# Performance work log

Measured on AMD Instinct MI355X. Metric: run time of the kernel, lower is better.

The kernel has to match this reference:

```python
import jax, jax.numpy as jnp
import numpy as np

P, H, T, B = 16, 24, 168, 4096


def _lstm(x, W_ih, W_hh, b_ih, b_hh):
    # x: [B, T, F]; PyTorch gate order i, f, g, o; returns all hidden states [B, T, H]
    Bsz = x.shape[0]
    Hd = W_hh.shape[1]
    # batch the input GEMM over all timesteps
    xg = jnp.einsum('btf,gf->btg', x, W_ih) + b_ih + b_hh  # [B, T, 4H]

    def step(carry, xt):
        h, c = carry
        g = xt + h @ W_hh.T  # [B, 4H]
        i, f, gg, o = jnp.split(g, 4, axis=-1)
        c = jax.nn.sigmoid(f) * c + jax.nn.sigmoid(i) * jnp.tanh(gg)
        h = jax.nn.sigmoid(o) * jnp.tanh(c)
        return (h, c), h

    h0 = jnp.zeros((Bsz, Hd), x.dtype)
    _, hs = jax.lax.scan(step, (h0, h0), jnp.swapaxes(xg, 0, 1))
    return jnp.swapaxes(hs, 0, 1)  # [B, T, H]


def setup_inputs() -> dict:
    key = jax.random.key(0)
    ks = jax.random.split(key, 14)
    s1 = 1.0 / np.sqrt(H)
    u = lambda k, shape: jax.random.uniform(k, shape, jnp.float32, -s1, s1)
    return {
        'x': jax.random.normal(ks[0], (B, T, P), jnp.float32),
        'W_ih1': u(ks[1], (4 * H, P)), 'W_hh1': u(ks[2], (4 * H, H)),
        'b_ih1': u(ks[3], (4 * H,)), 'b_hh1': u(ks[4], (4 * H,)),
        'W_ih2': u(ks[5], (4 * H, H)), 'W_hh2': u(ks[6], (4 * H, H)),
        'b_ih2': u(ks[7], (4 * H,)), 'b_hh2': u(ks[8], (4 * H,)),
        'W1': u(ks[9], (16, H)), 'b1': u(ks[10], (16,)),
        'W2': u(ks[11], (H, 16)), 'b2': u(ks[12], (H,)),
    }


def reference(x, W_ih1, W_hh1, b_ih1, b_hh1, W_ih2, W_hh2, b_ih2, b_hh2, W1, b1, W2, b2):
    h = jnp.tanh(_lstm(x, W_ih1, W_hh1, b_ih1, b_hh1))       # [B, T, H]
    h = jnp.tanh(_lstm(h, W_ih2, W_hh2, b_ih2, b_hh2))       # [B, T, H]
    h = h[:, -1, :]                                           # [B, H]
    h = jax.nn.relu(h @ W1.T + b1)                            # [B, 16]; dropout = identity (eval mode)
    out = h @ W2.T + b2                                       # [B, 24]
    return out.reshape(out.shape[0], -1, 1)                   # [B, 24, 1]
```

## Files before the change

kernel.cpp:

```cpp
#include <hip/hip_runtime.h>

constexpr int T = 168;
constexpr int P = 16;
constexpr int H = 24;

typedef float v2f __attribute__((ext_vector_type(2)));

__device__ __forceinline__ v2f mk2(float a, float b) { v2f r; r[0] = a; r[1] = b; return r; }
__device__ __forceinline__ v2f bc2(float a)          { v2f r; r[0] = a; r[1] = a; return r; }
__device__ __forceinline__ v2f pkfma(v2f a, v2f b, v2f c) {
    return __builtin_elementwise_fma(a, b, c);
}

__device__ __forceinline__ float rcp_f(float x) { return __builtin_amdgcn_rcpf(x); }
__device__ __forceinline__ float sigm_f(float x) { return rcp_f(1.f + __expf(-x)); }
__device__ __forceinline__ float tanh_fast(float x) {
    return fmaf(2.f, rcp_f(1.f + __expf(-2.f * x)), -1.f);
}

#define KEEP2(v) asm volatile("" : "+v"(v))
#define LDS_SYNC() asm volatile("s_waitcnt lgkmcnt(0)" ::: "memory")

#define PK4(acc_, v4_, w_, b_) do {                       \
    acc_ = pkfma(bc2((v4_).x), (w_)[(b_)],     acc_);     \
    acc_ = pkfma(bc2((v4_).y), (w_)[(b_) + 1], acc_);     \
    acc_ = pkfma(bc2((v4_).z), (w_)[(b_) + 2], acc_);     \
    acc_ = pkfma(bc2((v4_).w), (w_)[(b_) + 3], acc_); } while (0)

__device__ __forceinline__ void act_store(v2f g, int lane, int half,
                                          float& c, float* hdst, float* tdst)
{
    float a0 = sigm_f(g[0]);
    float px = (half == 0) ? g[1] + g[1] : g[1];
    float sv = sigm_f(px);
    float a1 = (half == 0) ? sv + sv - 1.f : sv;
    float fa = __shfl(a0, lane + 24);
    float oa = __shfl(a1, lane + 24);
    c = fmaf(fa, c, a0 * a1);
    float hv = oa * tanh_fast(c);
    if (tdst) {
        float th = tanh_fast(hv);
        if (lane < H) { hdst[lane] = hv; tdst[lane] = th; }
    } else {
        if (lane < H) hdst[lane] = hv;
    }
}

#define L1_STEP_L(xlsrow_, hrow_, c_, tdst_) do {                      \
    v2f g_ = bias;                                                     \
    _Pragma("unroll")                                                  \
    for (int j_ = 0; j_ < P / 4; ++j_) {                               \
        float4 v_ = ((const float4*)(xlsrow_))[j_];                    \
        PK4(g_, v_, w, 4 * j_);                                        \
    }                                                                  \
    _Pragma("unroll")                                                  \
    for (int k_ = 0; k_ < H / 4; ++k_) {                               \
        float4 hv_ = ((const float4*)(hrow_))[k_];                     \
        PK4(g_, hv_, w, H + 4 * k_);                                   \
    }                                                                  \
    act_store(g_, lane, half, c_, hrow_, tdst_);                       \
} while (0)

#define L2_STEP(trow_, hrow_, c_) do {                                 \
    v2f f_ = bias;                                                     \
    _Pragma("unroll")                                                  \
    for (int k_ = 0; k_ < H / 4; ++k_) {                               \
        float4 tv_ = ((const float4*)(trow_))[k_];                     \
        PK4(f_, tv_, w, 4 * k_);                                       \
    }                                                                  \
    _Pragma("unroll")                                                  \
    for (int k_ = 0; k_ < H / 4; ++k_) {                               \
        float4 hv_ = ((const float4*)(hrow_))[k_];                     \
        PK4(f_, hv_, w, H + 4 * k_);                                   \
    }                                                                  \
    act_store(f_, lane, half, c_, hrow_, nullptr);                     \
} while (0)

__global__ __attribute__((amdgpu_flat_work_group_size(128, 128),
                          amdgpu_num_vgpr(128)))
void lstm2_split6(const float* __restrict__ x,
                  const float* __restrict__ Wih1, const float* __restrict__ Whh1,
                  const float* __restrict__ bih1, const float* __restrict__ bhh1,
                  const float* __restrict__ Wih2, const float* __restrict__ Whh2,
                  const float* __restrict__ bih2, const float* __restrict__ bhh2,
                  const float* __restrict__ W1, const float* __restrict__ b1,
                  const float* __restrict__ W2, const float* __restrict__ b2,
                  float* __restrict__ out)
{
    const int tid  = threadIdx.x;
    const int wid  = tid >> 6;
    const int lane = tid & 63;
    const int s    = (lane < 48) ? lane : 47;
    const int u    = s % H;
    const int half = s / H;
    const int q0   = half * H + u;
    const int q1   = (2 + half) * H + u;
    const int rowA = blockIdx.x * 2;
    const int rowB = rowA + 1;

    const float* __restrict__ Wi = wid ? Wih2 : Wih1;
    const float* __restrict__ Wh = wid ? Whh2 : Whh1;
    const float* __restrict__ bi = wid ? bih2 : bih1;
    const float* __restrict__ bh = wid ? bhh2 : bhh1;
    const int nin = wid ? H : P;

    v2f w[48];
    #pragma unroll
    for (int k = 0; k < H; ++k)
        w[k] = (k < nin) ? mk2(Wi[q0 * nin + k], Wi[q1 * nin + k]) : bc2(0.f);
    #pragma unroll
    for (int k = 0; k < H; ++k)
        w[H + k] = mk2(Wh[q0 * H + k], Wh[q1 * H + k]);
    v2f bias = mk2(bi[q0] + bh[q0], bi[q1] + bh[q1]);

    #pragma unroll
    for (int k = 0; k < 48; ++k) KEEP2(w[k]);
    KEEP2(bias);

    __shared__ __align__(16) float h1s[2][32];
    __shared__ __align__(16) float t1s[2][2][2][32];
    __shared__ __align__(16) float h2s[2][32];
    __shared__ __align__(16) float xls[2][2][8][16];

    const float* __restrict__ xA = x + (size_t)rowA * T * P;
    const float* __restrict__ xB = x + (size_t)rowB * T * P;

    float cA = 0.f, cB = 0.f;

    const int xr  = lane >> 5;
    const int xo4 = lane & 31;
    const float* __restrict__ xbase = xr ? xB : xA;
    float4 xst;

    if (wid == 0) {
        xst = ((const float4*)xbase)[xo4];
        ((float4*)xls[0][xr])[xo4] = xst;
        xst = ((const float4*)(xbase + 128))[xo4];
        LDS_SYNC();

        {
            v2f g = bias;
            #pragma unroll
            for (int j = 0; j < P / 4; ++j) {
                float4 v = ((const float4*)xls[0][0][0])[j];
                PK4(g, v, w, 4 * j);
            }
            act_store(g, lane, half, cA, h1s[0], t1s[0][0][0]);
        }
        {
            v2f g = bias;
            #pragma unroll
            for (int j = 0; j < P / 4; ++j) {
                float4 v = ((const float4*)xls[0][1][0])[j];
                PK4(g, v, w, 4 * j);
            }
            act_store(g, lane, half, cB, h1s[1], t1s[0][0][1]);
        }
        LDS_SYNC();
        L1_STEP_L(xls[0][0][1], h1s[0], cA, t1s[0][1][0]);
        L1_STEP_L(xls[0][1][1], h1s[1], cB, t1s[0][1][1]);
    } else {
        if (lane < H) { h2s[0][lane] = 0.f; h2s[1][lane] = 0.f; }
    }
    LDS_SYNC();
    __builtin_amdgcn_s_barrier();

    for (int ss = 1; ss < T / 2; ++ss) {
        if (wid == 0) {
            if ((ss & 3) == 0) {
                const int ci = ss >> 2;
                ((float4*)xls[ci & 1][xr])[xo4] = xst;
                if (ci < 20)
                    xst = ((const float4*)(xbase + (ci + 1) * 128))[xo4];
                LDS_SYNC();
            }
            const int xb = (ss >> 2) & 1;
            const int ta = 2 * ss;
            L1_STEP_L(xls[xb][0][ta & 7],       h1s[0], cA, t1s[ss & 1][0][0]);
            L1_STEP_L(xls[xb][1][ta & 7],       h1s[1], cB, t1s[ss & 1][0][1]);
            LDS_SYNC();
            L1_STEP_L(xls[xb][0][(ta + 1) & 7], h1s[0], cA, t1s[ss & 1][1][0]);
            L1_STEP_L(xls[xb][1][(ta + 1) & 7], h1s[1], cB, t1s[ss & 1][1][1]);
        } else {
            const int pb = (ss - 1) & 1;
            L2_STEP(t1s[pb][0][0], h2s[0], cA);
            L2_STEP(t1s[pb][0][1], h2s[1], cB);
            LDS_SYNC();
            L2_STEP(t1s[pb][1][0], h2s[0], cA);
            L2_STEP(t1s[pb][1][1], h2s[1], cB);
        }
        LDS_SYNC();
        __builtin_amdgcn_s_barrier();
    }

    if (wid == 1) {
        L2_STEP(t1s[1][0][0], h2s[0], cA);
        L2_STEP(t1s[1][0][1], h2s[1], cB);
        LDS_SYNC();
        L2_STEP(t1s[1][1][0], h2s[0], cA);
        L2_STEP(t1s[1][1][1], h2s[1], cB);
        LDS_SYNC();

        if (lane < H) {
            t1s[0][0][0][lane] = tanh_fast(h2s[0][lane]);
            t1s[0][0][1][lane] = tanh_fast(h2s[1][lane]);
        }
        LDS_SYNC();
        if (lane < 16) {
            float accA = b1[lane], accB = b1[lane];
            #pragma unroll
            for (int j = 0; j < H; ++j) {
                float wv = W1[lane * H + j];
                accA = fmaf(t1s[0][0][0][j], wv, accA);
                accB = fmaf(t1s[0][0][1][j], wv, accB);
            }
            h1s[0][lane] = fmaxf(accA, 0.f);
            h1s[1][lane] = fmaxf(accB, 0.f);
        }
        LDS_SYNC();
        if (lane < H) {
            float accA = b2[lane], accB = b2[lane];
            #pragma unroll
            for (int j = 0; j < 16; ++j) {
                float wv = W2[lane * 16 + j];
                accA = fmaf(h1s[0][j], wv, accA);
                accB = fmaf(h1s[1][j], wv, accB);
            }
            out[(size_t)rowA * H + lane] = accA;
            out[(size_t)rowB * H + lane] = accB;
        }
    }
}

extern "C" void kernel_launch(void* const* d_in, const int* in_sizes, int n_in,
                              void* d_out, int out_size, void* d_ws, size_t ws_size,
                              hipStream_t stream)
{
    const float* x    = (const float*)d_in[0];
    const float* Wih1 = (const float*)d_in[1];
    const float* Whh1 = (const float*)d_in[2];
    const float* bih1 = (const float*)d_in[3];
    const float* bhh1 = (const float*)d_in[4];
    const float* Wih2 = (const float*)d_in[5];
    const float* Whh2 = (const float*)d_in[6];
    const float* bih2 = (const float*)d_in[7];
    const float* bhh2 = (const float*)d_in[8];
    const float* W1   = (const float*)d_in[9];
    const float* b1   = (const float*)d_in[10];
    const float* W2   = (const float*)d_in[11];
    const float* b2   = (const float*)d_in[12];
    float* out = (float*)d_out;

    const int B = in_sizes[0] / (T * P);
    hipLaunchKernelGGL(lstm2_split6, dim3(B / 2), dim3(128), 0, stream,
                       x, Wih1, Whh1, bih1, bhh1, Wih2, Whh2, bih2, bhh2,
                       W1, b1, W2, b2, out);
}
```

Baseline: 405.0 us.

## Keep LSTM hidden state in registers and broadcast via readlane instead of LDS

The recurrent hidden states for both layers now stay in a VGPR per lane, and each matvec broadcasts h elements with v_readlane into scalar operands, replacing the LDS round-trip (store h, waitcnt, float4 reloads) on the serial critical path. Layer 2 also reads its tanh(h1) input with one LDS load per lane and broadcasts it through readlane. This removes intermediate LDS waits between steps but adds 24–48 readlane instructions per step, which may serialize on the scalar path.

```diff
diff --git a/kernel.cpp b/kernel.cpp
--- a/kernel.cpp
+++ b/kernel.cpp
@@ -16,6 +16,11 @@
 __device__ __forceinline__ float sigm_f(float x) { return rcp_f(1.f + __expf(-x)); }
 __device__ __forceinline__ float tanh_fast(float x) {
     return fmaf(2.f, rcp_f(1.f + __expf(-2.f * x)), -1.f);
+}
+
+__device__ __forceinline__ float rdlane(float v, int k) {
+    return __builtin_bit_cast(float,
+        __builtin_amdgcn_readlane(__builtin_bit_cast(int, v), k));
 }
 
 #define KEEP2(v) asm volatile("" : "+v"(v))
@@ -27,8 +32,7 @@
     acc_ = pkfma(bc2((v4_).z), (w_)[(b_) + 2], acc_);     \
     acc_ = pkfma(bc2((v4_).w), (w_)[(b_) + 3], acc_); } while (0)
 
-__device__ __forceinline__ void act_store(v2f g, int lane, int half,
-                                          float& c, float* hdst, float* tdst)
+__device__ __forceinline__ float act_update(v2f g, int lane, int half, float& c)
 {
     float a0 = sigm_f(g[0]);
     float px = (half == 0) ? g[1] + g[1] : g[1];
@@ -37,16 +41,10 @@
     float fa = __shfl(a0, lane + 24);
     float oa = __shfl(a1, lane + 24);
     c = fmaf(fa, c, a0 * a1);
-    float hv = oa * tanh_fast(c);
-    if (tdst) {
-        float th = tanh_fast(hv);
-        if (lane < H) { hdst[lane] = hv; tdst[lane] = th; }
-    } else {
-        if (lane < H) hdst[lane] = hv;
-    }
-}
-
-#define L1_STEP_L(xlsrow_, hrow_, c_, tdst_) do {                      \
+    return oa * tanh_fast(c);
+}
+
+#define L1S(xlsrow_, hreg_, c_, tdst_) do {                            \
     v2f g_ = bias;                                                     \
     _Pragma("unroll")                                                  \
     for (int j_ = 0; j_ < P / 4; ++j_) {                               \
@@ -54,31 +52,28 @@
         PK4(g_, v_, w, 4 * j_);                                        \
     }                                                                  \
     _Pragma("unroll")                                                  \
-    for (int k_ = 0; k_ < H / 4; ++k_) {                               \
-        float4 hv_ = ((const float4*)(hrow_))[k_];                     \
-        PK4(g_, hv_, w, H + 4 * k_);                                   \
-    }                                                                  \
-    act_store(g_, lane, half, c_, hrow_, tdst_);                       \
+    for (int k_ = 0; k_ < H; ++k_)                                     \
+        g_ = pkfma(bc2(rdlane(hreg_, k_)), w[H + k_], g_);             \
+    hreg_ = act_update(g_, lane, half, c_);                            \
+    float th_ = tanh_fast(hreg_);                                      \
+    if (lane < H) (tdst_)[lane] = th_;                                 \
 } while (0)
 
-#define L2_STEP(trow_, hrow_, c_) do {                                 \
+#define L2S(tsrc_, hreg_, c_) do {                                     \
+    float tv_ = (tsrc_)[lane & 31];                                    \
     v2f f_ = bias;                                                     \
     _Pragma("unroll")                                                  \
-    for (int k_ = 0; k_ < H / 4; ++k_) {                               \
-        float4 tv_ = ((const float4*)(trow_))[k_];                     \
-        PK4(f_, tv_, w, 4 * k_);                                       \
-    }                                                                  \
-    _Pragma("unroll")                                                  \
-    for (int k_ = 0; k_ < H / 4; ++k_) {                               \
-        float4 hv_ = ((const float4*)(hrow_))[k_];                     \
-        PK4(f_, hv_, w, H + 4 * k_);                                   \
-    }                                                                  \
-    act_store(f_, lane, half, c_, hrow_, nullptr);                     \
+    for (int k_ = 0; k_ < H; ++k_)                                     \
+        f_ = pkfma(bc2(rdlane(tv_, k_)), w[k_], f_);                   \
+    _Pragma("unroll")                                                  \
+    for (int k_ = 0; k_ < H; ++k_)                                     \
+        f_ = pkfma(bc2(rdlane(hreg_, k_)), w[H + k_], f_);             \
+    hreg_ = act_update(f_, lane, half, c_);                            \
 } while (0)
 
 __global__ __attribute__((amdgpu_flat_work_group_size(128, 128),
                           amdgpu_num_vgpr(128)))
-void lstm2_split6(const float* __restrict__ x,
+void lstm2_split7(const float* __restrict__ x,
                   const float* __restrict__ Wih1, const float* __restrict__ Whh1,
                   const float* __restrict__ bih1, const float* __restrict__ bhh1,
                   const float* __restrict__ Wih2, const float* __restrict__ Whh2,
@@ -117,15 +112,14 @@
     for (int k = 0; k < 48; ++k) KEEP2(w[k]);
     KEEP2(bias);
 
-    __shared__ __align__(16) float h1s[2][32];
     __shared__ __align__(16) float t1s[2][2][2][32];
-    __shared__ __align__(16) float h2s[2][32];
     __shared__ __align__(16) float xls[2][2][8][16];
 
     const float* __restrict__ xA = x + (size_t)rowA * T * P;
     const float* __restrict__ xB = x + (size_t)rowB * T * P;
 
     float cA = 0.f, cB = 0.f;
+    float hA = 0.f, hB = 0.f;
 
     const int xr  = lane >> 5;
     const int xo4 = lane & 31;
@@ -137,30 +131,10 @@
         ((float4*)xls[0][xr])[xo4] = xst;
         xst = ((const float4*)(xbase + 128))[xo4];
         LDS_SYNC();
-
-        {
-            v2f g = bias;
-            #pragma unroll
-            for (int j = 0; j < P / 4; ++j) {
-                float4 v = ((const float4*)xls[0][0][0])[j];
-                PK4(g, v, w, 4 * j);
-            }
-            act_store(g, lane, half, cA, h1s[0], t1s[0][0][0]);
-        }
-        {
-            v2f g = bias;
-            #pragma unroll
-            for (int j = 0; j < P / 4; ++j) {
-                float4 v = ((const float4*)xls[0][1][0])[j];
-                PK4(g, v, w, 4 * j);
-            }
-            act_store(g, lane, half, cB, h1s[1], t1s[0][0][1]);
-        }
-        LDS_SYNC();
-        L1_STEP_L(xls[0][0][1], h1s[0], cA, t1s[0][1][0]);
-        L1_STEP_L(xls[0][1][1], h1s[1], cB, t1s[0][1][1]);
-    } else {
-        if (lane < H) { h2s[0][lane] = 0.f; h2s[1][lane] = 0.f; }
+        L1S(xls[0][0][0], hA, cA, t1s[0][0][0]);
+        L1S(xls[0][1][0], hB, cB, t1s[0][0][1]);
+        L1S(xls[0][0][1], hA, cA, t1s[0][1][0]);
+        L1S(xls[0][1][1], hB, cB, t1s[0][1][1]);
     }
     LDS_SYNC();
     __builtin_amdgcn_s_barrier();
@@ -176,34 +150,30 @@
             }
             const int xb = (ss >> 2) & 1;
             const int ta = 2 * ss;
-            L1_STEP_L(xls[xb][0][ta & 7],       h1s[0], cA, t1s[ss & 1][0][0]);
-            L1_STEP_L(xls[xb][1][ta & 7],       h1s[1], cB, t1s[ss & 1][0][1]);
-            LDS_SYNC();
-            L1_STEP_L(xls[xb][0][(ta + 1) & 7], h1s[0], cA, t1s[ss & 1][1][0]);
-            L1_STEP_L(xls[xb][1][(ta + 1) & 7], h1s[1], cB, t1s[ss & 1][1][1]);
+            L1S(xls[xb][0][ta & 7],       hA, cA, t1s[ss & 1][0][0]);
+            L1S(xls[xb][1][ta & 7],       hB, cB, t1s[ss & 1][0][1]);
+            L1S(xls[xb][0][(ta + 1) & 7], hA, cA, t1s[ss & 1][1][0]);
+            L1S(xls[xb][1][(ta + 1) & 7], hB, cB, t1s[ss & 1][1][1]);
         } else {
             const int pb = (ss - 1) & 1;
-            L2_STEP(t1s[pb][0][0], h2s[0], cA);
-            L2_STEP(t1s[pb][0][1], h2s[1], cB);
-            LDS_SYNC();
-            L2_STEP(t1s[pb][1][0], h2s[0], cA);
-            L2_STEP(t1s[pb][1][1], h2s[1], cB);
+            L2S(t1s[pb][0][0], hA, cA);
+            L2S(t1s[pb][0][1], hB, cB);
+            L2S(t1s[pb][1][0], hA, cA);
+            L2S(t1s[pb][1][1], hB, cB);
         }
         LDS_SYNC();
         __builtin_amdgcn_s_barrier();
     }
 
     if (wid == 1) {
-        L2_STEP(t1s[1][0][0], h2s[0], cA);
-        L2_STEP(t1s[1][0][1], h2s[1], cB);
-        LDS_SYNC();
-        L2_STEP(t1s[1][1][0], h2s[0], cA);
-        L2_STEP(t1s[1][1][1], h2s[1], cB);
-        LDS_SYNC();
+        L2S(t1s[1][0][0], hA, cA);
+        L2S(t1s[1][0][1], hB, cB);
+        L2S(t1s[1][1][0], hA, cA);
+        L2S(t1s[1][1][1], hB, cB);
 
         if (lane < H) {
-            t1s[0][0][0][lane] = tanh_fast(h2s[0][lane]);
-            t1s[0][0][1][lane] = tanh_fast(h2s[1][lane]);
+            t1s[0][0][0][lane] = tanh_fast(hA);
+            t1s[0][0][1][lane] = tanh_fast(hB);
         }
         LDS_SYNC();
         if (lane < 16) {
@@ -214,8 +184,8 @@
                 accA = fmaf(t1s[0][0][0][j], wv, accA);
                 accB = fmaf(t1s[0][0][1][j], wv, accB);
             }
-            h1s[0][lane] = fmaxf(accA, 0.f);
-            h1s[1][lane] = fmaxf(accB, 0.f);
+            t1s[0][1][0][lane] = fmaxf(accA, 0.f);
+            t1s[0][1][1][lane] = fmaxf(accB, 0.f);
         }
         LDS_SYNC();
         if (lane < H) {
@@ -223,8 +193,8 @@
             #pragma unroll
             for (int j = 0; j < 16; ++j) {
                 float wv = W2[lane * 16 + j];
-                accA = fmaf(h1s[0][j], wv, accA);
-                accB = fmaf(h1s[1][j], wv, accB);
+                accA = fmaf(t1s[0][1][0][j], wv, accA);
+                accB = fmaf(t1s[0][1][1][j], wv, accB);
             }
             out[(size_t)rowA * H + lane] = accA;
             out[(size_t)rowB * H + lane] = accB;
@@ -252,7 +222,7 @@
     float* out = (float*)d_out;
 
     const int B = in_sizes[0] / (T * P);
-    hipLaunchKernelGGL(lstm2_split6, dim3(B / 2), dim3(128), 0, stream,
+    hipLaunchKernelGGL(lstm2_split7, dim3(B / 2), dim3(128), 0, stream,
                        x, Wih1, Whh1, bih1, bhh1, Wih2, Whh2, bih2, bhh2,
                        W1, b1, W2, b2, out);
 }
```

After: 486.6 us. 20.1% more time.
